# Kernel optimization log

Hardware: AMD Instinct MI355X
Metric: run time of the kernel (lower is better)

Reference implementation:

```python
import jax, jax.numpy as jnp
import numpy as np

N, L, H, D = 4, 2048, 16, 32   # batch, seq len, heads, projection_dim
DIM = H * D                     # 512 model dim


def setup_inputs() -> dict:
    rng = jax.random.key(0)
    k1, k2, k3, k4, k5 = jax.random.split(rng, 5)
    query = jax.random.normal(k1, (N, L, DIM), dtype=jnp.float32)
    key = jax.random.normal(k2, (N, L, DIM), dtype=jnp.float32)
    scale = 0.02
    Wq = jax.random.normal(k3, (DIM, DIM), dtype=jnp.float32) * scale
    Wk = jax.random.normal(k4, (DIM, DIM), dtype=jnp.float32) * scale
    Wv = jax.random.normal(k5, (DIM, DIM), dtype=jnp.float32) * scale
    return {"query": query, "key": key, "Wq": Wq, "Wk": Wk, "Wv": Wv, "mask": 1}


def reference(query, key, Wq, Wk, Wv, mask):
    # torch Linear(bias=False): y = x @ W^T
    n, Lq, _ = query.shape
    _, Lk, _ = key.shape
    q = (query @ Wq.T).reshape(n, Lq, H, D).transpose(0, 2, 1, 3)  # (N,H,Lq,D)
    k = (key @ Wk.T).reshape(n, Lk, H, D).transpose(0, 2, 1, 3)    # (N,H,Lk,D)
    v = (key @ Wv.T).reshape(n, Lk, H, D).transpose(0, 2, 1, 3)    # (N,H,Lk,D)
    q = jax.nn.softmax(q, axis=-1)
    k = jax.nn.softmax(k, axis=-1)
    # causal branch (mask truthy): Lq*Lk > D^2*Lk, so the module takes the
    # cumsum-of-outer-products ("right") path:
    #   right = cumsum_l( k_l outer v_l );  out_l = q_l @ right_l
    kv = jnp.einsum('nhld,nhle->nhlde', k, v)   # (N,H,Lk,D,D) outer products
    S = jnp.cumsum(kv, axis=2)                  # running prefix state
    out = jnp.einsum('nhld,nhlde->nhle', q, S)  # (N,H,Lq,D)
    return out.transpose(0, 2, 1, 3).reshape(n, Lq, H * D)
```

## Files before the change

### kernel.cpp

```cpp
#include <hip/hip_runtime.h>

#define NB      4
#define L_SEQ   2048
#define H_HEADS 16
#define D32     32
#define DIM     512
#define NH      (NB * H_HEADS)
#define CHUNK   64
#define NCHUNK  (L_SEQ / CHUNK)

typedef __attribute__((ext_vector_type(8))) short bf16x8;
typedef __attribute__((ext_vector_type(4))) float f32x4;

__device__ __forceinline__ unsigned short f2bf(float x) {
    unsigned u = __float_as_uint(x);
    u += 0x7fff + ((u >> 16) & 1);
    return (unsigned short)(u >> 16);
}
__device__ __forceinline__ unsigned pack2(float lo, float hi) {
    return (unsigned)f2bf(lo) | ((unsigned)f2bf(hi) << 16);
}

#define QN  4194304
#define WN  262144
#define TOT (2*QN + 3*WN)
__global__ __launch_bounds__(256) void convert_kernel(
    const float* __restrict__ query, const float* __restrict__ key,
    const float* __restrict__ Wq, const float* __restrict__ Wk,
    const float* __restrict__ Wv, unsigned short* __restrict__ dst)
{
    int idx = (blockIdx.x * 256 + threadIdx.x) * 8;
    const float* src; int off;
    if (idx < QN)               { src = query; off = idx; }
    else if (idx < 2*QN)        { src = key;   off = idx - QN; }
    else if (idx < 2*QN + WN)   { src = Wq;    off = idx - 2*QN; }
    else if (idx < 2*QN + 2*WN) { src = Wk;    off = idx - 2*QN - WN; }
    else                        { src = Wv;    off = idx - 2*QN - 2*WN; }
    float4 a = *(const float4*)(src + off);
    float4 b = *(const float4*)(src + off + 4);
    *(uint4*)(dst + idx) = make_uint4(pack2(a.x, a.y), pack2(a.z, a.w),
                                      pack2(b.x, b.y), pack2(b.z, b.w));
}

__global__ __launch_bounds__(256) void gemm3_mfma_kernel(
    const unsigned short* __restrict__ qb, const unsigned short* __restrict__ kb2,
    const unsigned short* __restrict__ wqb, const unsigned short* __restrict__ wkb,
    const unsigned short* __restrict__ wvb,
    unsigned short* __restrict__ Qs, unsigned short* __restrict__ Ks,
    unsigned short* __restrict__ Vt)
{
    const int z = blockIdx.z;
    const unsigned short *PA, *PB;
    int m0, n0;
    if (z == 0)      { PA = qb;  PB = wqb; m0 = blockIdx.y*128; n0 = blockIdx.x*128; }
    else if (z == 1) { PA = kb2; PB = wkb; m0 = blockIdx.y*128; n0 = blockIdx.x*128; }
    else             { PA = wvb; PB = kb2; m0 = blockIdx.x*128; n0 = blockIdx.y*128; }

    __shared__ unsigned short Asm[128 * 32];
    __shared__ unsigned short Bsm[128 * 32];

    const int t    = threadIdx.x;
    const int w    = t >> 6;
    const int lane = t & 63;
    const int wm   = w >> 1, wn = w & 1;
    const int chunkoff = ((lane & 15) * 4 + (lane >> 4)) * 8;

    f32x4 acc[4][4] = {};

    for (int kb = 0; kb < DIM; kb += 32) {
        #pragma unroll
        for (int rep = 0; rep < 2; rep++) {
            int li  = t + rep * 256;
            int row = li >> 2, kq = li & 3;
            uint4 av = *(const uint4*)(PA + (size_t)(m0 + row) * DIM + kb + kq * 8);
            uint4 bv = *(const uint4*)(PB + (size_t)(n0 + row) * DIM + kb + kq * 8);
            ((uint4*)Asm)[li] = av;
            ((uint4*)Bsm)[li] = bv;
        }
        __syncthreads();

        bf16x8 af[4], bfr[4];
        #pragma unroll
        for (int i = 0; i < 4; i++)
            af[i] = *(const bf16x8*)(Asm + (wm * 4 + i) * 512 + chunkoff);
        #pragma unroll
        for (int j = 0; j < 4; j++)
            bfr[j] = *(const bf16x8*)(Bsm + (wn * 4 + j) * 512 + chunkoff);
        #pragma unroll
        for (int i = 0; i < 4; i++)
            #pragma unroll
            for (int j = 0; j < 4; j++)
                acc[i][j] = __builtin_amdgcn_mfma_f32_16x16x32_bf16(
                    af[i], bfr[j], acc[i][j], 0, 0, 0);
        __syncthreads();
    }

    if (z < 2) {
        #pragma unroll
        for (int i = 0; i < 4; i++)
            #pragma unroll
            for (int jp = 0; jp < 2; jp++)
                #pragma unroll
                for (int r = 0; r < 4; r++) {
                    float a = acc[i][2 * jp][r], b = acc[i][2 * jp + 1][r];
                    float m = fmaxf(a, b);
                    #pragma unroll
                    for (int off = 1; off < 16; off <<= 1)
                        m = fmaxf(m, __shfl_xor(m, off, 64));
                    float ea = __expf(a - m), eb = __expf(b - m);
                    float s = ea + eb;
                    #pragma unroll
                    for (int off = 1; off < 16; off <<= 1)
                        s += __shfl_xor(s, off, 64);
                    float inv = 1.0f / s;
                    acc[i][2 * jp][r]     = ea * inv;
                    acc[i][2 * jp + 1][r] = eb * inv;
                }
    }

    const int quad = lane >> 4, lm = lane & 15;
    #pragma unroll
    for (int i = 0; i < 4; i++) {
        int rbase = m0 + wm * 64 + i * 16 + quad * 4;
        #pragma unroll
        for (int r = 0; r < 4; r++) {
            int rg = rbase + r;
            #pragma unroll
            for (int j = 0; j < 4; j++) {
                int cg = n0 + wn * 64 + j * 16 + lm;
                unsigned short val = f2bf(acc[i][j][r]);
                if (z < 2) {
                    int n = rg >> 11, l = rg & 2047;
                    int h = cg >> 5,  e = cg & 31;
                    unsigned short* dp = (z == 0) ? Qs : Ks;
                    dp[(((size_t)(n * H_HEADS + h)) * L_SEQ + l) * D32 + e] = val;
                } else {
                    int h = rg >> 5,  e = rg & 31;
                    int n = cg >> 11, l = cg & 2047;
                    Vt[(((size_t)(n * H_HEADS + h)) * D32 + e) * L_SEQ + l] = val;
                }
            }
        }
    }
}

__global__ __launch_bounds__(256) void chunk_kv_mfma_kernel(
    const unsigned short* __restrict__ Ks, const unsigned short* __restrict__ Vt,
    float* __restrict__ ckvT)
{
    const int nh = blockIdx.y;
    const int t  = threadIdx.x;
    const int w  = t >> 6;
    const int c  = blockIdx.x * 4 + w;
    const int lane = t & 63;
    const int lm = lane & 15, quad = lane >> 4;

    __shared__ unsigned short Kl[4 * 64 * 36];

    {
        const unsigned short* kg = Ks + ((size_t)nh * L_SEQ + blockIdx.x * 4 * CHUNK) * D32;
        #pragma unroll
        for (int rr = 0; rr < 4; rr++) {
            int gi = t + rr * 256;
            int lrow = gi >> 2, kq = gi & 3;
            uint4 v = *(const uint4*)(kg + (size_t)lrow * D32 + kq * 8);
            *(uint4*)(Kl + lrow * 36 + kq * 8) = v;
        }
    }
    __syncthreads();

    f32x4 acc[2][2] = {};
    #pragma unroll
    for (int ch = 0; ch < 2; ch++) {
        bf16x8 aV[2], bK[2];
        #pragma unroll
        for (int mt = 0; mt < 2; mt++)
            aV[mt] = *(const bf16x8*)(Vt + ((size_t)nh * D32 + mt * 16 + lm) * L_SEQ
                                         + c * CHUNK + ch * 32 + quad * 8);
        #pragma unroll
        for (int nt = 0; nt < 2; nt++) {
            const unsigned short* kp = Kl + (w * 64 + ch * 32 + quad * 8) * 36
                                          + nt * 16 + lm;
            #pragma unroll
            for (int j = 0; j < 8; j++) bK[nt][j] = (short)kp[j * 36];
        }
        #pragma unroll
        for (int mt = 0; mt < 2; mt++)
            #pragma unroll
            for (int nt = 0; nt < 2; nt++)
                acc[mt][nt] = __builtin_amdgcn_mfma_f32_16x16x32_bf16(
                    aV[mt], bK[nt], acc[mt][nt], 0, 0, 0);
    }
    #pragma unroll
    for (int mt = 0; mt < 2; mt++)
        #pragma unroll
        for (int nt = 0; nt < 2; nt++)
            #pragma unroll
            for (int r = 0; r < 4; r++) {
                int e = mt * 16 + quad * 4 + r;
                int d = nt * 16 + lm;
                ckvT[(((size_t)nh * NCHUNK + c) * 32 + e) * 32 + d] = acc[mt][nt][r];
            }
}

__global__ __launch_bounds__(256) void prefix_kernel(
    const float* __restrict__ ckvT, unsigned short* __restrict__ SpT)
{
    int nh = blockIdx.x;
    int t  = threadIdx.x;
    const float* base = ckvT + (size_t)nh * NCHUNK * 1024 + t * 4;
    unsigned short* sp = SpT + (size_t)nh * NCHUNK * 1024 + t * 4;
    float4 acc = make_float4(0.f, 0.f, 0.f, 0.f);
    #pragma unroll
    for (int cb = 0; cb < NCHUNK; cb += 8) {
        float4 v[8];
        #pragma unroll
        for (int j = 0; j < 8; j++)
            v[j] = *(const float4*)(base + (size_t)(cb + j) * 1024);
        #pragma unroll
        for (int j = 0; j < 8; j++) {
            ushort4 u;
            u.x = f2bf(acc.x); u.y = f2bf(acc.y);
            u.z = f2bf(acc.z); u.w = f2bf(acc.w);
            *(ushort4*)(sp + (size_t)(cb + j) * 1024) = u;
            acc.x += v[j].x; acc.y += v[j].y;
            acc.z += v[j].z; acc.w += v[j].w;
        }
    }
}

__global__ __launch_bounds__(256) void chunk_out_mfma_kernel(
    const unsigned short* __restrict__ Qs, const unsigned short* __restrict__ Ks,
    const unsigned short* __restrict__ Vt, const unsigned short* __restrict__ SpT,
    float* __restrict__ out)
{
    const int c = blockIdx.x, nh = blockIdx.y;
    __shared__ unsigned short P[64 * 72];

    const int t = threadIdx.x, w = t >> 6, lane = t & 63;
    const int lm = lane & 15, quad = lane >> 4;

    bf16x8 aQ = *(const bf16x8*)(Qs + ((size_t)nh * L_SEQ + c * CHUNK + w * 16 + lm) * D32
                                    + quad * 8);

    #pragma unroll
    for (int j = 0; j < 4; j++) {
        f32x4 p = {};
        if (j <= w) {
            bf16x8 bK = *(const bf16x8*)(Ks + ((size_t)nh * L_SEQ + c * CHUNK + j * 16 + lm) * D32
                                            + quad * 8);
            p = __builtin_amdgcn_mfma_f32_16x16x32_bf16(aQ, bK, p, 0, 0, 0);
            if (j == w) {
                #pragma unroll
                for (int r = 0; r < 4; r++)
                    if (lm > quad * 4 + r) p[r] = 0.f;
            }
        }
        #pragma unroll
        for (int r = 0; r < 4; r++)
            P[(w * 16 + quad * 4 + r) * 72 + j * 16 + lm] = f2bf(p[r]);
    }
    __syncthreads();

    const int chains = (w < 2) ? 1 : 2;
    bf16x8 aP[2];
    for (int ch = 0; ch < chains; ch++)
        aP[ch] = *(const bf16x8*)&P[(w * 16 + lm) * 72 + ch * 32 + quad * 8];

    const int n = nh >> 4, h = nh & 15;
    #pragma unroll
    for (int nt = 0; nt < 2; nt++) {
        bf16x8 bS = *(const bf16x8*)(SpT + (((size_t)nh * NCHUNK + c) * 32 + nt * 16 + lm) * 32
                                         + quad * 8);
        f32x4 acc = {};
        acc = __builtin_amdgcn_mfma_f32_16x16x32_bf16(aQ, bS, acc, 0, 0, 0);
        for (int ch = 0; ch < chains; ch++) {
            bf16x8 bV = *(const bf16x8*)(Vt + ((size_t)nh * D32 + nt * 16 + lm) * L_SEQ
                                            + c * CHUNK + ch * 32 + quad * 8);
            acc = __builtin_amdgcn_mfma_f32_16x16x32_bf16(aP[ch], bV, acc, 0, 0, 0);
        }
        #pragma unroll
        for (int r = 0; r < 4; r++) {
            int lg = c * CHUNK + w * 16 + quad * 4 + r;
            out[((size_t)n * L_SEQ + lg) * DIM + h * D32 + nt * 16 + lm] = acc[r];
        }
    }
}

extern "C" void kernel_launch(void* const* d_in, const int* in_sizes, int n_in,
                              void* d_out, int out_size, void* d_ws, size_t ws_size,
                              hipStream_t stream)
{
    (void)in_sizes; (void)n_in; (void)out_size; (void)ws_size;
    const float* query = (const float*)d_in[0];
    const float* key   = (const float*)d_in[1];
    const float* Wq    = (const float*)d_in[2];
    const float* Wk    = (const float*)d_in[3];
    const float* Wv    = (const float*)d_in[4];
    float* out = (float*)d_out;

    unsigned short* bf = (unsigned short*)d_ws;
    unsigned short* qb  = bf;
    unsigned short* kb  = qb + QN;
    unsigned short* wqb = kb + QN;
    unsigned short* wkb = wqb + WN;
    unsigned short* wvb = wkb + WN;
    unsigned short* Qs  = wvb + WN;
    const size_t SZ = (size_t)NH * L_SEQ * D32;
    unsigned short* Ks  = Qs + SZ;
    unsigned short* Vt  = Ks + SZ;
    unsigned short* SpT = Vt + SZ;
    float* ckvT = (float*)(SpT + (size_t)NH * NCHUNK * 1024);

    dim3 blk(256);
    convert_kernel<<<dim3(TOT / (256 * 8)), blk, 0, stream>>>(query, key, Wq, Wk, Wv, qb);
    gemm3_mfma_kernel<<<dim3(4, 64, 3), blk, 0, stream>>>(qb, kb, wqb, wkb, wvb,
                                                          Qs, Ks, Vt);
    chunk_kv_mfma_kernel<<<dim3(NCHUNK / 4, NH), blk, 0, stream>>>(Ks, Vt, ckvT);
    prefix_kernel<<<dim3(NH), blk, 0, stream>>>(ckvT, SpT);
    chunk_out_mfma_kernel<<<dim3(NCHUNK, NH), blk, 0, stream>>>(Qs, Ks, Vt, SpT, out);
}
```

Baseline: 166.0 us.

## Rework block shapes: single-wave blocks for chunk kernels, split prefix scan

Changes the work decomposition of several kernels. chunk_kv now uses one 64-thread block per chunk instead of four chunks per 256-thread block. prefix is split across 4 blocks per head so more CUs take part. chunk_out has one wavefront handle a whole 64-row chunk, so per-wave causal imbalance is replaced by a sequential loop over four row tiles. The GEMM grid is flattened so consecutive blocks share the same weight column tile. The aim is more parallelism in the tiny prefix kernel and better L2 reuse, at the cost of more small blocks and more serial work per wave in chunk_out.

```diff
diff --git a/kernel.cpp b/kernel.cpp
--- a/kernel.cpp
+++ b/kernel.cpp
@@ -49,12 +49,14 @@
     unsigned short* __restrict__ Qs, unsigned short* __restrict__ Ks,
     unsigned short* __restrict__ Vt)
 {
-    const int z = blockIdx.z;
+    const int z  = blockIdx.z;
+    const int bx = blockIdx.x >> 6;
+    const int by = blockIdx.x & 63;
     const unsigned short *PA, *PB;
     int m0, n0;
-    if (z == 0)      { PA = qb;  PB = wqb; m0 = blockIdx.y*128; n0 = blockIdx.x*128; }
-    else if (z == 1) { PA = kb2; PB = wkb; m0 = blockIdx.y*128; n0 = blockIdx.x*128; }
-    else             { PA = wvb; PB = kb2; m0 = blockIdx.x*128; n0 = blockIdx.y*128; }
+    if (z == 0)      { PA = qb;  PB = wqb; m0 = by*128; n0 = bx*128; }
+    else if (z == 1) { PA = kb2; PB = wkb; m0 = by*128; n0 = bx*128; }
+    else             { PA = wvb; PB = kb2; m0 = bx*128; n0 = by*128; }
 
     __shared__ unsigned short Asm[128 * 32];
     __shared__ unsigned short Bsm[128 * 32];
@@ -144,27 +146,22 @@
     }
 }
 
-__global__ __launch_bounds__(256) void chunk_kv_mfma_kernel(
+__global__ __launch_bounds__(64) void chunk_kv_mfma_kernel(
     const unsigned short* __restrict__ Ks, const unsigned short* __restrict__ Vt,
     float* __restrict__ ckvT)
 {
-    const int nh = blockIdx.y;
-    const int t  = threadIdx.x;
-    const int w  = t >> 6;
-    const int c  = blockIdx.x * 4 + w;
-    const int lane = t & 63;
+    const int c = blockIdx.x, nh = blockIdx.y;
+    const int lane = threadIdx.x;
     const int lm = lane & 15, quad = lane >> 4;
 
-    __shared__ unsigned short Kl[4 * 64 * 36];
+    __shared__ unsigned short Kl[64 * 36];
 
     {
-        const unsigned short* kg = Ks + ((size_t)nh * L_SEQ + blockIdx.x * 4 * CHUNK) * D32;
-        #pragma unroll
-        for (int rr = 0; rr < 4; rr++) {
-            int gi = t + rr * 256;
-            int lrow = gi >> 2, kq = gi & 3;
-            uint4 v = *(const uint4*)(kg + (size_t)lrow * D32 + kq * 8);
-            *(uint4*)(Kl + lrow * 36 + kq * 8) = v;
+        const unsigned short* kg = Ks + ((size_t)nh * L_SEQ + c * CHUNK + lane) * D32;
+        #pragma unroll
+        for (int i = 0; i < 4; i++) {
+            uint4 v = *(const uint4*)(kg + i * 8);
+            *(uint4*)(Kl + lane * 36 + i * 8) = v;
         }
     }
     __syncthreads();
@@ -179,8 +176,7 @@
                                          + c * CHUNK + ch * 32 + quad * 8);
         #pragma unroll
         for (int nt = 0; nt < 2; nt++) {
-            const unsigned short* kp = Kl + (w * 64 + ch * 32 + quad * 8) * 36
-                                          + nt * 16 + lm;
+            const unsigned short* kp = Kl + (ch * 32 + quad * 8) * 36 + nt * 16 + lm;
             #pragma unroll
             for (int j = 0; j < 8; j++) bK[nt][j] = (short)kp[j * 36];
         }
@@ -203,13 +199,13 @@
             }
 }
 
-__global__ __launch_bounds__(256) void prefix_kernel(
+__global__ __launch_bounds__(64) void prefix_kernel(
     const float* __restrict__ ckvT, unsigned short* __restrict__ SpT)
 {
-    int nh = blockIdx.x;
-    int t  = threadIdx.x;
-    const float* base = ckvT + (size_t)nh * NCHUNK * 1024 + t * 4;
-    unsigned short* sp = SpT + (size_t)nh * NCHUNK * 1024 + t * 4;
+    int nh   = blockIdx.y;
+    int slot = blockIdx.x * 64 + threadIdx.x;
+    const float* base = ckvT + (size_t)nh * NCHUNK * 1024 + slot * 4;
+    unsigned short* sp = SpT + (size_t)nh * NCHUNK * 1024 + slot * 4;
     float4 acc = make_float4(0.f, 0.f, 0.f, 0.f);
     #pragma unroll
     for (int cb = 0; cb < NCHUNK; cb += 8) {
@@ -229,7 +225,7 @@
     }
 }
 
-__global__ __launch_bounds__(256) void chunk_out_mfma_kernel(
+__global__ __launch_bounds__(64) void chunk_out_mfma_kernel(
     const unsigned short* __restrict__ Qs, const unsigned short* __restrict__ Ks,
     const unsigned short* __restrict__ Vt, const unsigned short* __restrict__ SpT,
     float* __restrict__ out)
@@ -237,52 +233,68 @@
     const int c = blockIdx.x, nh = blockIdx.y;
     __shared__ unsigned short P[64 * 72];
 
-    const int t = threadIdx.x, w = t >> 6, lane = t & 63;
+    const int lane = threadIdx.x;
     const int lm = lane & 15, quad = lane >> 4;
 
-    bf16x8 aQ = *(const bf16x8*)(Qs + ((size_t)nh * L_SEQ + c * CHUNK + w * 16 + lm) * D32
+    bf16x8 aQ[4], bK[4];
+    #pragma unroll
+    for (int i = 0; i < 4; i++)
+        aQ[i] = *(const bf16x8*)(Qs + ((size_t)nh * L_SEQ + c * CHUNK + i * 16 + lm) * D32
                                     + quad * 8);
-
-    #pragma unroll
-    for (int j = 0; j < 4; j++) {
-        f32x4 p = {};
-        if (j <= w) {
-            bf16x8 bK = *(const bf16x8*)(Ks + ((size_t)nh * L_SEQ + c * CHUNK + j * 16 + lm) * D32
-                                            + quad * 8);
-            p = __builtin_amdgcn_mfma_f32_16x16x32_bf16(aQ, bK, p, 0, 0, 0);
-            if (j == w) {
-                #pragma unroll
-                for (int r = 0; r < 4; r++)
-                    if (lm > quad * 4 + r) p[r] = 0.f;
+    #pragma unroll
+    for (int j = 0; j < 4; j++)
+        bK[j] = *(const bf16x8*)(Ks + ((size_t)nh * L_SEQ + c * CHUNK + j * 16 + lm) * D32
+                                    + quad * 8);
+
+    #pragma unroll
+    for (int i = 0; i < 4; i++) {
+        #pragma unroll
+        for (int j = 0; j < 4; j++) {
+            f32x4 p = {};
+            if (j <= i) {
+                p = __builtin_amdgcn_mfma_f32_16x16x32_bf16(aQ[i], bK[j], p, 0, 0, 0);
+                if (j == i) {
+                    #pragma unroll
+                    for (int r = 0; r < 4; r++)
+                        if (lm > quad * 4 + r) p[r] = 0.f;
+                }
             }
-        }
-        #pragma unroll
-        for (int r = 0; r < 4; r++)
-            P[(w * 16 + quad * 4 + r) * 72 + j * 16 + lm] = f2bf(p[r]);
+            #pragma unroll
+            for (int r = 0; r < 4; r++)
+                P[(i * 16 + quad * 4 + r) * 72 + j * 16 + lm] = f2bf(p[r]);
+        }
     }
     __syncthreads();
 
-    const int chains = (w < 2) ? 1 : 2;
-    bf16x8 aP[2];
-    for (int ch = 0; ch < chains; ch++)
-        aP[ch] = *(const bf16x8*)&P[(w * 16 + lm) * 72 + ch * 32 + quad * 8];
+    bf16x8 bS[2], bV[2][2];
+    #pragma unroll
+    for (int nt = 0; nt < 2; nt++) {
+        bS[nt] = *(const bf16x8*)(SpT + (((size_t)nh * NCHUNK + c) * 32 + nt * 16 + lm) * 32
+                                      + quad * 8);
+        #pragma unroll
+        for (int ch = 0; ch < 2; ch++)
+            bV[nt][ch] = *(const bf16x8*)(Vt + ((size_t)nh * D32 + nt * 16 + lm) * L_SEQ
+                                             + c * CHUNK + ch * 32 + quad * 8);
+    }
 
     const int n = nh >> 4, h = nh & 15;
     #pragma unroll
-    for (int nt = 0; nt < 2; nt++) {
-        bf16x8 bS = *(const bf16x8*)(SpT + (((size_t)nh * NCHUNK + c) * 32 + nt * 16 + lm) * 32
-                                         + quad * 8);
-        f32x4 acc = {};
-        acc = __builtin_amdgcn_mfma_f32_16x16x32_bf16(aQ, bS, acc, 0, 0, 0);
-        for (int ch = 0; ch < chains; ch++) {
-            bf16x8 bV = *(const bf16x8*)(Vt + ((size_t)nh * D32 + nt * 16 + lm) * L_SEQ
-                                            + c * CHUNK + ch * 32 + quad * 8);
-            acc = __builtin_amdgcn_mfma_f32_16x16x32_bf16(aP[ch], bV, acc, 0, 0, 0);
-        }
-        #pragma unroll
-        for (int r = 0; r < 4; r++) {
-            int lg = c * CHUNK + w * 16 + quad * 4 + r;
-            out[((size_t)n * L_SEQ + lg) * DIM + h * D32 + nt * 16 + lm] = acc[r];
+    for (int i = 0; i < 4; i++) {
+        const int chmax = (i >> 1) + 1;
+        bf16x8 aP[2];
+        for (int ch = 0; ch < chmax; ch++)
+            aP[ch] = *(const bf16x8*)&P[(i * 16 + lm) * 72 + ch * 32 + quad * 8];
+        #pragma unroll
+        for (int nt = 0; nt < 2; nt++) {
+            f32x4 acc = {};
+            acc = __builtin_amdgcn_mfma_f32_16x16x32_bf16(aQ[i], bS[nt], acc, 0, 0, 0);
+            for (int ch = 0; ch < chmax; ch++)
+                acc = __builtin_amdgcn_mfma_f32_16x16x32_bf16(aP[ch], bV[nt][ch], acc, 0, 0, 0);
+            #pragma unroll
+            for (int r = 0; r < 4; r++) {
+                int lg = c * CHUNK + i * 16 + quad * 4 + r;
+                out[((size_t)n * L_SEQ + lg) * DIM + h * D32 + nt * 16 + lm] = acc[r];
+            }
         }
     }
 }
@@ -312,11 +324,11 @@
     unsigned short* SpT = Vt + SZ;
     float* ckvT = (float*)(SpT + (size_t)NH * NCHUNK * 1024);
 
-    dim3 blk(256);
-    convert_kernel<<<dim3(TOT / (256 * 8)), blk, 0, stream>>>(query, key, Wq, Wk, Wv, qb);
-    gemm3_mfma_kernel<<<dim3(4, 64, 3), blk, 0, stream>>>(qb, kb, wqb, wkb, wvb,
-                                                          Qs, Ks, Vt);
-    chunk_kv_mfma_kernel<<<dim3(NCHUNK / 4, NH), blk, 0, stream>>>(Ks, Vt, ckvT);
-    prefix_kernel<<<dim3(NH), blk, 0, stream>>>(ckvT, SpT);
-    chunk_out_mfma_kernel<<<dim3(NCHUNK, NH), blk, 0, stream>>>(Qs, Ks, Vt, SpT, out);
-}
+    convert_kernel<<<dim3(TOT / (256 * 8)), dim3(256), 0, stream>>>(
+        query, key, Wq, Wk, Wv, qb);
+    gemm3_mfma_kernel<<<dim3(256, 1, 3), dim3(256), 0, stream>>>(
+        qb, kb, wqb, wkb, wvb, Qs, Ks, Vt);
+    chunk_kv_mfma_kernel<<<dim3(NCHUNK, NH), dim3(64), 0, stream>>>(Ks, Vt, ckvT);
+    prefix_kernel<<<dim3(4, NH), dim3(64), 0, stream>>>(ckvT, SpT);
+    chunk_out_mfma_kernel<<<dim3(NCHUNK, NH), dim3(64), 0, stream>>>(Qs, Ks, Vt, SpT, out);
+}
```

Result: faster. 140.8 us (-15.2%).
